# Performance work log

Hardware: AMD Instinct MI355X
Metric: run time of the kernel (lower is better)

Reference implementation:

```python
import jax, jax.numpy as jnp
import numpy as np

N = 50000      # nodes
E = 400000     # edges
HID = 128      # hidden_size
L = 3          # num_att_layer
K = 9          # rbf_size
H = 4          # heads
C = HID // H   # out_channels per head (32)
G = 512        # graphs in batch
CUTOFF = 10.0


def _rbf(D):
    # ExponentialRBF: softplus(softplus_inverse(x)) == x, so centers/widths are the raw values
    centers = jnp.linspace(1.0, float(np.exp(-CUTOFF)), K)          # (K,)
    width = (0.5 / ((1.0 - np.exp(-CUTOFF)) / K)) ** 2              # scalar
    x = D / CUTOFF
    x3 = x ** 3
    x4 = x3 * x
    x5 = x4 * x
    cut = jnp.where(x < 1.0, 1.0 - 6.0 * x5 + 15.0 * x4 - 10.0 * x3, 0.0)
    return cut[:, None] * jnp.exp(-width * (jnp.exp(-D)[:, None] - centers) ** 2)  # (E,K)


def _ln(x, g, b):
    mu = jnp.mean(x, axis=-1, keepdims=True)
    var = jnp.var(x, axis=-1, keepdims=True)
    return (x - mu) / jnp.sqrt(var + 1e-5) * g + b


def _seg_softmax(logits, seg, n):
    # numerically stable softmax over edges grouped by target node
    m = jax.ops.segment_max(logits, seg, num_segments=n)
    e = jnp.exp(logits - m[seg])
    s = jax.ops.segment_sum(e, seg, num_segments=n)
    return e / s[seg]


def setup_inputs() -> dict:
    key = jax.random.key(0)
    ks = jax.random.split(key, 32)
    s = 1.0 / np.sqrt(HID)
    se = 1.0 / np.sqrt(K + 1)
    sb = 1.0 / np.sqrt(3 * HID)
    nrm = jax.random.normal
    inp = {
        "h": nrm(ks[0], (N, HID), jnp.float32),
        "pos": nrm(ks[1], (N, 3), jnp.float32) * 3.0,
        "edge_weight": jax.random.uniform(ks[2], (E,), jnp.float32),
        "Wq": nrm(ks[3], (L, HID, HID)) * s,   "bq": nrm(ks[4], (L, HID)) * 0.01,
        "Wk": nrm(ks[5], (L, HID, HID)) * s,   "bk": nrm(ks[6], (L, HID)) * 0.01,
        "Wv": nrm(ks[7], (L, HID, HID)) * s,   "bv": nrm(ks[8], (L, HID)) * 0.01,
        "We": nrm(ks[9], (L, K + 1, HID)) * se,
        "Wskip": nrm(ks[10], (L, HID, HID)) * s, "bskip": nrm(ks[11], (L, HID)) * 0.01,
        "Wbeta": nrm(ks[12], (L, 3 * HID, 1)) * sb,
        "Wffn1": nrm(ks[13], (L, HID, HID)) * s, "bffn1": nrm(ks[14], (L, HID)) * 0.01,
        "Wffn2": nrm(ks[15], (L, HID, HID)) * s, "bffn2": nrm(ks[16], (L, HID)) * 0.01,
        "Wffn3": nrm(ks[17], (L, HID, HID)) * s, "bffn3": nrm(ks[18], (L, HID)) * 0.01,
        "ln_g": jnp.ones((HID,), jnp.float32),
        "ln_b": jnp.zeros((HID,), jnp.float32),
        "Wo1": nrm(ks[19], (HID, HID)) * s, "bo1": nrm(ks[20], (HID,)) * 0.01,
        "Wo2": nrm(ks[21], (HID, 1)) * s,   "bo2": nrm(ks[22], (1,)) * 0.01,
        "edge_index": jax.random.randint(ks[23], (2, E), 0, N),
        "batch": jnp.sort(jax.random.randint(ks[24], (N,), 0, G)),
    }
    return inp


def reference(h, pos, edge_weight, Wq, bq, Wk, bk, Wv, bv, We, Wskip, bskip, Wbeta,
              Wffn1, bffn1, Wffn2, bffn2, Wffn3, bffn3, ln_g, ln_b, Wo1, bo1, Wo2, bo2,
              edge_index, batch):
    sp = jax.nn.softplus
    n = h.shape[0]
    src, dst = edge_index[0], edge_index[1]  # source j -> target i
    D = jnp.linalg.norm(pos[dst] - pos[src], axis=-1)              # (E,)
    efeat = jnp.concatenate([_rbf(D), edge_weight[:, None]], -1)   # (E, K+1)
    inv_sqrt_c = 1.0 / np.sqrt(C)

    for i in range(L):
        hn = _ln(h, ln_g, ln_b)
        q = (hn @ Wq[i] + bq[i]).reshape(n, H, C)
        k = (hn @ Wk[i] + bk[i]).reshape(n, H, C)
        v = (hn @ Wv[i] + bv[i]).reshape(n, H, C)
        ea = (efeat @ We[i]).reshape(-1, H, C)                     # (E,H,C)
        kj = k[src] + ea
        alpha = jnp.einsum('ehc,ehc->eh', q[dst], kj) * inv_sqrt_c  # (E,H)
        alpha = _seg_softmax(alpha, dst, n)
        # dropout p=0.5 is a no-op in eval mode
        msg = (v[src] + ea) * alpha[:, :, None]
        out = jax.ops.segment_sum(msg, dst, num_segments=n).reshape(n, H * C)
        x_r = hn @ Wskip[i] + bskip[i]
        beta = jax.nn.sigmoid(jnp.concatenate([out, x_r, out - x_r], -1) @ Wbeta[i])
        out = beta * x_r + (1.0 - beta) * out
        h = hn + sp(out)
        hn2 = _ln(h, ln_g, ln_b)
        f = sp(hn2 @ Wffn1[i] + bffn1[i])
        f = sp(f @ Wffn2[i] + bffn2[i])
        f = sp(f @ Wffn3[i] + bffn3[i])
        h = hn2 + f

    pooled = jax.ops.segment_sum(h, batch, num_segments=G)          # (G, HID)
    return sp(pooled @ Wo1 + bo1) @ Wo2 + bo2                       # (G, 1)
```

## Files before the change

### kernel.cpp

```cpp
#include <hip/hip_runtime.h>
#include <hip/hip_bf16.h>
#include <math.h>

#define HID 128
#define KRBF 9
#define NLAYER 3
#define QSSTR 320
#define KVSTR 256
#define QWCOLS 576

typedef __attribute__((ext_vector_type(8))) short bf16x8;
typedef __attribute__((ext_vector_type(4))) float f32x4;

__device__ __forceinline__ float sp_(float x){ return fmaxf(x,0.f) + log1pf(expf(-fabsf(x))); }
__device__ __forceinline__ float sigm_(float x){ return 1.f/(1.f+expf(-x)); }
__device__ __forceinline__ float b2f(short s){
  union{unsigned u; float f;} x; x.u = ((unsigned)(unsigned short)s)<<16; return x.f;
}
__device__ __forceinline__ float wsum64(float v){
  #pragma unroll
  for(int m=1;m<64;m<<=1) v += __shfl_xor(v,m,64);
  return v;
}
__device__ __forceinline__ float wsum16(float v){
  #pragma unroll
  for(int m=1;m<16;m<<=1) v += __shfl_xor(v,m,64);
  return v;
}
__device__ __forceinline__ float2 ldbf2(const __hip_bfloat16* p){
  __hip_bfloat162 b = *(const __hip_bfloat162*)p;
  return make_float2(__bfloat162float(b.x), __bfloat162float(b.y));
}
__device__ __forceinline__ int lb_(const int* __restrict__ a, int n, int key){
  int lo=0, hi=n;
  while(lo<hi){ int mid=(lo+hi)>>1; if(a[mid]<key) lo=mid+1; else hi=mid; }
  return lo;
}

__global__ void count_dst(const int* __restrict__ ei, int* __restrict__ counts, int E){
  int e = blockIdx.x*256+threadIdx.x;
  if(e<E) atomicAdd(&counts[ei[E+e]],1);
}
__global__ void scan1(const int* __restrict__ counts, int* __restrict__ tmp,
                      int* __restrict__ bsums, int N){
  __shared__ int lds[256];
  int t = threadIdx.x; int idx = blockIdx.x*256+t;
  int v = (idx<N)? counts[idx]:0;
  lds[t]=v; __syncthreads();
  for(int off=1;off<256;off<<=1){
    int x = (t>=off)? lds[t-off]:0;
    __syncthreads();
    lds[t]+=x; __syncthreads();
  }
  if(idx<N) tmp[idx]=lds[t];
  if(t==255) bsums[blockIdx.x]=lds[255];
}
__global__ void scan2(const int* __restrict__ bsums, int* __restrict__ boffs, int nb){
  __shared__ int lds[256];
  int t=threadIdx.x;
  int v = (t<nb)? bsums[t]:0;
  lds[t]=v; __syncthreads();
  for(int off=1;off<256;off<<=1){
    int x=(t>=off)?lds[t-off]:0;
    __syncthreads();
    lds[t]+=x; __syncthreads();
  }
  if(t<nb) boffs[t] = lds[t]-v;
}
__global__ void finalize_rs(const int* __restrict__ tmp, const int* __restrict__ boffs,
                            int* __restrict__ row_start, int N){
  int idx = blockIdx.x*256+threadIdx.x;
  if(idx<N) row_start[idx+1] = tmp[idx] + boffs[idx>>8];
  if(idx==0) row_start[0]=0;
}

__global__ void edge_prep(const float* __restrict__ pos, const float* __restrict__ ew,
                          const int* __restrict__ ei, const int* __restrict__ rowst,
                          int* __restrict__ counts2, float* __restrict__ efs,
                          int* __restrict__ esrc, int E){
  int e = blockIdx.x*256 + threadIdx.x;
  if(e>=E) return;
  int s = ei[e], d = ei[E+e];
  float dx = pos[d*3+0]-pos[s*3+0];
  float dy = pos[d*3+1]-pos[s*3+1];
  float dz = pos[d*3+2]-pos[s*3+2];
  float D = sqrtf(dx*dx+dy*dy+dz*dz);
  float x = D*0.1f;
  float cut = 0.f;
  if(x < 1.f){ float x3=x*x*x, x4=x3*x, x5=x4*x; cut = 1.f - 6.f*x5 + 15.f*x4 - 10.f*x3; }
  float ed = expf(-D);
  const double e10 = 4.5399929762484854e-05;
  const float step  = (float)((e10 - 1.0)/8.0);
  const float width = (float)((4.5/(1.0-e10))*(4.5/(1.0-e10)));
  float r12[12];
  #pragma unroll
  for(int k=0;k<KRBF;k++){
    float c = 1.0f + k*step;
    float dd = ed - c;
    r12[k] = cut*expf(-width*dd*dd);
  }
  r12[9] = ew[e]; r12[10]=0.f; r12[11]=0.f;
  int p = rowst[d] + atomicAdd(&counts2[d],1);
  float* o = efs + (size_t)p*12;
  *(float4*)&o[0] = *(float4*)&r12[0];
  *(float4*)&o[4] = *(float4*)&r12[4];
  *(float4*)&o[8] = *(float4*)&r12[8];
  esrc[p] = s;
}

__global__ void pack_w(const float* __restrict__ Wq, const float* __restrict__ Wk,
                       const float* __restrict__ Wv, const float* __restrict__ Wsk,
                       const float* __restrict__ bq, const float* __restrict__ bk,
                       const float* __restrict__ bv, const float* __restrict__ bsk,
                       const float* __restrict__ We,
                       const float* __restrict__ W1, const float* __restrict__ W2,
                       const float* __restrict__ W3,
                       __hip_bfloat16* __restrict__ Wqkvs, float* __restrict__ bqkvs,
                       __hip_bfloat16* __restrict__ Wffn){
  int idx = blockIdx.x*256 + threadIdx.x;
  const int QT = NLAYER*QWCOLS*128;
  const int FT = NLAYER*3*128*128;
  const int BT = NLAYER*QWCOLS;
  if(idx < QT){
    int l = idx / (QWCOLS*128);
    int rem = idx - l*(QWCOLS*128);
    int col = rem >> 7, k = rem & 127;
    float v;
    if(col < 512){
      const float* src = (col<128)?Wq:((col<256)?Wk:((col<384)?Wv:Wsk));
      v = src[(size_t)l*16384 + k*128 + (col&127)];
    } else if(col < 552){
      int j = col-512; int h=j/10; int r=j-10*h;
      const float* wq = Wq + (size_t)l*16384 + k*128;
      const float* we = We + (size_t)l*1280 + r*128;
      float acc=0.f;
      #pragma unroll 8
      for(int c=32*h;c<32*h+32;c++) acc = fmaf(wq[c], we[c], acc);
      v = acc;
    } else v = 0.f;
    Wqkvs[idx] = __float2bfloat16(v);
  } else if(idx < QT+FT){
    int j = idx - QT;
    int k = j & 127; int n = (j>>7)&127; int f = (j>>14)%3; int l = j/(3*16384);
    const float* src = (f==0)?W1:((f==1)?W2:W3);
    Wffn[j] = __float2bfloat16(src[(size_t)l*16384 + k*128 + n]);
  } else if(idx < QT+FT+BT){
    int j = idx - QT - FT;
    int l = j/QWCOLS; int col = j - l*QWCOLS;
    float v;
    if(col<512){
      const float* src = (col<128)?bq:((col<256)?bk:((col<384)?bv:bsk));
      v = src[l*128 + (col&127)];
    } else if(col<552){
      int jj=col-512; int h=jj/10; int r=jj-10*h;
      const float* bqp = bq + l*128;
      const float* we = We + (size_t)l*1280 + r*128;
      float acc=0.f;
      for(int c=32*h;c<32*h+32;c++) acc = fmaf(bqp[c], we[c], acc);
      v = acc;
    } else v = 0.f;
    bqkvs[j] = v;
  }
}

__global__ void ln_node(const float* __restrict__ h, const float* __restrict__ g,
                        const float* __restrict__ b, __hip_bfloat16* __restrict__ hn, int N){
  int n = blockIdx.x*4 + (threadIdx.x>>6);
  if(n>=N) return;
  int lane = threadIdx.x & 63;
  int c = 2*lane;
  float2 v = *(const float2*)&h[(size_t)n*HID + c];
  float s1 = wsum64(v.x+v.y);
  float s2 = wsum64(v.x*v.x+v.y*v.y);
  float mu = s1*(1.f/HID);
  float var = s2*(1.f/HID) - mu*mu;
  float rs = rsqrtf(var + 1e-5f);
  __hip_bfloat162 o;
  o.x = __float2bfloat16((v.x-mu)*rs*g[c]   + b[c]);
  o.y = __float2bfloat16((v.y-mu)*rs*g[c+1] + b[c+1]);
  *(__hip_bfloat162*)&hn[(size_t)n*HID + c] = o;
}

__global__ __launch_bounds__(256) void gemm_mfma(
    const __hip_bfloat16* __restrict__ A, const __hip_bfloat16* __restrict__ Wt,
    const float* __restrict__ bias, const __hip_bfloat16* __restrict__ res,
    void* __restrict__ out0, void* __restrict__ out1,
    const float* __restrict__ lng, const float* __restrict__ lnb,
    int N, int ncols, int mode){
  __shared__ __hip_bfloat16 As[128][136];
  __shared__ __hip_bfloat16 Ws[128][136];
  int row0 = blockIdx.y*128;
  int col0 = blockIdx.x*128;
  int tid = threadIdx.x;
  {
    int chunk = tid&15; int rbase = tid>>4;
    #pragma unroll
    for(int i=0;i<8;i++){
      int r = rbase + 16*i;
      int row = row0 + r;
      float4 v = make_float4(0.f,0.f,0.f,0.f);
      if(row < N) v = *(const float4*)&A[(size_t)row*128 + chunk*8];
      *(float4*)&As[r][chunk*8] = v;
    }
    #pragma unroll
    for(int i=0;i<8;i++){
      int c = rbase + 16*i;
      float4 v = make_float4(0.f,0.f,0.f,0.f);
      if(col0 + c < ncols) v = *(const float4*)&Wt[(size_t)(col0+c)*128 + chunk*8];
      *(float4*)&Ws[c][chunk*8] = v;
    }
  }
  __syncthreads();
  int lane = tid&63;
  int m0 = (tid>>6)*32;
  int ql = lane>>4;
  int il = lane&15;
  f32x4 acc[2][8];
  #pragma unroll
  for(int mi=0;mi<2;mi++)
    #pragma unroll
    for(int nj=0;nj<8;nj++)
      acc[mi][nj] = (f32x4){0.f,0.f,0.f,0.f};
  #pragma unroll
  for(int kk=0;kk<128;kk+=32){
    bf16x8 a0 = *(bf16x8*)&As[m0+il][kk+ql*8];
    bf16x8 a1 = *(bf16x8*)&As[m0+16+il][kk+ql*8];
    bf16x8 bb[8];
    #pragma unroll
    for(int nj=0;nj<8;nj++) bb[nj] = *(bf16x8*)&Ws[nj*16+il][kk+ql*8];
    #pragma unroll
    for(int nj=0;nj<8;nj++){
      acc[0][nj] = __builtin_amdgcn_mfma_f32_16x16x32_bf16(a0, bb[nj], acc[0][nj], 0,0,0);
      acc[1][nj] = __builtin_amdgcn_mfma_f32_16x16x32_bf16(a1, bb[nj], acc[1][nj], 0,0,0);
    }
  }
  if(mode==0){
    __hip_bfloat16* qs  = (__hip_bfloat16*)out0;
    __hip_bfloat16* kvb = (__hip_bfloat16*)out1;
    #pragma unroll
    for(int mi=0;mi<2;mi++){
      int rowb = row0 + m0 + mi*16 + ql*4;
      #pragma unroll
      for(int r=0;r<4;r++){
        int rr = rowb + r;
        if(rr >= N) continue;
        #pragma unroll
        for(int nj=0;nj<8;nj++){
          int cg = col0 + nj*16 + il;
          if(cg >= QWCOLS) continue;
          float t = acc[mi][nj][r] + bias[cg];
          __hip_bfloat16 bv = __float2bfloat16(t);
          if(cg < 128)      qs[(size_t)rr*QSSTR + cg] = bv;
          else if(cg < 384) kvb[(size_t)rr*KVSTR + (cg-128)] = bv;
          else if(cg < 512) qs[(size_t)rr*QSSTR + 128 + (cg-384)] = bv;
          else if(cg < 552) qs[(size_t)rr*QSSTR + 256 + (cg-512)] = bv;
        }
      }
    }
  } else if(mode==1){
    __hip_bfloat16* o = (__hip_bfloat16*)out0;
    #pragma unroll
    for(int mi=0;mi<2;mi++){
      int rowb = row0 + m0 + mi*16 + ql*4;
      #pragma unroll
      for(int r=0;r<4;r++){
        int rr = rowb + r;
        if(rr >= N) continue;
        #pragma unroll
        for(int nj=0;nj<8;nj++){
          int cg = nj*16 + il;
          o[(size_t)rr*128 + cg] = __float2bfloat16(sp_(acc[mi][nj][r] + bias[cg]));
        }
      }
    }
  } else {
    float* hout = (float*)out0;
    __hip_bfloat16* hnout = (__hip_bfloat16*)out1;
    #pragma unroll
    for(int mi=0;mi<2;mi++){
      int rowb = row0 + m0 + mi*16 + ql*4;
      float t[8][4];
      #pragma unroll
      for(int r=0;r<4;r++){
        int rr = rowb + r;
        bool ok = rr < N;
        #pragma unroll
        for(int nj=0;nj<8;nj++){
          int cg = nj*16 + il;
          float x = sp_(acc[mi][nj][r] + bias[cg]);
          float rv = ok ? __bfloat162float(res[(size_t)rr*128 + cg]) : 0.f;
          t[nj][r] = x + rv;
        }
      }
      #pragma unroll
      for(int r=0;r<4;r++){
        int rr = rowb + r;
        if(rr >= N) continue;
        float s1=0.f, s2=0.f;
        #pragma unroll
        for(int nj=0;nj<8;nj++){ float v=t[nj][r]; s1+=v; s2+=v*v; }
        s1 = wsum16(s1); s2 = wsum16(s2);
        float mu = s1*(1.f/128.f);
        float var = s2*(1.f/128.f) - mu*mu;
        float rs = rsqrtf(var + 1e-5f);
        #pragma unroll
        for(int nj=0;nj<8;nj++){
          int cg = nj*16 + il;
          float tv = t[nj][r];
          hout[(size_t)rr*128 + cg] = tv;
          hnout[(size_t)rr*128 + cg] = __float2bfloat16((tv-mu)*rs*lng[cg] + lnb[cg]);
        }
      }
    }
  }
}

__global__ __launch_bounds__(256) void attn_fused2(
    const __hip_bfloat16* __restrict__ qs, const __hip_bfloat16* __restrict__ kvb,
    const float* __restrict__ efs, const int* __restrict__ esrc,
    const float* __restrict__ WeL, const int* __restrict__ rowst,
    float* __restrict__ att, int N){
  int n = blockIdx.x*4 + (threadIdx.x>>6);
  if(n>=N) return;
  int lane = threadIdx.x & 63;
  int eg = lane>>4, sl = lane&15;
  int c8 = sl*8, hd = sl>>2;
  const __hip_bfloat16* rowq = qs + (size_t)n*QSSTR;
  float q8[8];
  {
    bf16x8 qv = *(const bf16x8*)&rowq[c8];
    #pragma unroll
    for(int j=0;j<8;j++) q8[j] = b2f(qv[j]);
  }
  float QW[10];
  #pragma unroll
  for(int r=0;r<10;r++) QW[r] = __bfloat162float(rowq[256 + hd*10 + r]);
  int lo = rowst[n], hi = rowst[n+1];
  float ssum = 0.f;
  float a8[8]; float S[10];
  #pragma unroll
  for(int j=0;j<8;j++) a8[j]=0.f;
  #pragma unroll
  for(int r=0;r<10;r++) S[r]=0.f;
  int i = lo + eg;
  if(i < hi){
    int s = esrc[i];
    const __hip_bfloat16* kr = kvb + (size_t)s*KVSTR;
    bf16x8 kc = *(const bf16x8*)&kr[c8];
    bf16x8 vc = *(const bf16x8*)&kr[128 + c8];
    const float* ef = efs + (size_t)i*12;
    float4 e0 = *(const float4*)&ef[0];
    float4 e1 = *(const float4*)&ef[4];
    float2 e2 = *(const float2*)&ef[8];
    while(true){
      int inext = i + 4;
      bool more = inext < hi;
      bf16x8 kn = kc, vn = vc;
      float4 f0 = e0, f1 = e1; float2 f2 = e2;
      if(more){
        int s2 = esrc[inext];
        const __hip_bfloat16* kr2 = kvb + (size_t)s2*KVSTR;
        kn = *(const bf16x8*)&kr2[c8];
        vn = *(const bf16x8*)&kr2[128 + c8];
        const float* ef2 = efs + (size_t)inext*12;
        f0 = *(const float4*)&ef2[0];
        f1 = *(const float4*)&ef2[4];
        f2 = *(const float2*)&ef2[8];
      }
      float d = 0.f;
      #pragma unroll
      for(int j=0;j<8;j++) d = fmaf(q8[j], b2f(kc[j]), d);
      d += __shfl_xor(d,1,64); d += __shfl_xor(d,2,64);
      float lg = d;
      lg = fmaf(e0.x,QW[0],lg); lg = fmaf(e0.y,QW[1],lg);
      lg = fmaf(e0.z,QW[2],lg); lg = fmaf(e0.w,QW[3],lg);
      lg = fmaf(e1.x,QW[4],lg); lg = fmaf(e1.y,QW[5],lg);
      lg = fmaf(e1.z,QW[6],lg); lg = fmaf(e1.w,QW[7],lg);
      lg = fmaf(e2.x,QW[8],lg); lg = fmaf(e2.y,QW[9],lg);
      lg *= 0.17677669529663687f;
      lg = fminf(lg, 80.f);
      float w = __expf(lg);
      ssum += w;
      #pragma unroll
      for(int j=0;j<8;j++) a8[j] = fmaf(w, b2f(vc[j]), a8[j]);
      S[0]=fmaf(w,e0.x,S[0]); S[1]=fmaf(w,e0.y,S[1]); S[2]=fmaf(w,e0.z,S[2]);
      S[3]=fmaf(w,e0.w,S[3]); S[4]=fmaf(w,e1.x,S[4]); S[5]=fmaf(w,e1.y,S[5]);
      S[6]=fmaf(w,e1.z,S[6]); S[7]=fmaf(w,e1.w,S[7]); S[8]=fmaf(w,e2.x,S[8]);
      S[9]=fmaf(w,e2.y,S[9]);
      if(!more) break;
      kc = kn; vc = vn; e0 = f0; e1 = f1; e2 = f2;
      i = inext;
    }
  }
  #pragma unroll
  for(int m=16;m<64;m<<=1){
    ssum += __shfl_xor(ssum,m,64);
    #pragma unroll
    for(int j=0;j<8;j++) a8[j] += __shfl_xor(a8[j],m,64);
    #pragma unroll
    for(int r=0;r<10;r++) S[r] += __shfl_xor(S[r],m,64);
  }
  float inv = (hi>lo)? 1.f/ssum : 0.f;
  float o8[8];
  #pragma unroll
  for(int j=0;j<8;j++) o8[j]=a8[j];
  #pragma unroll
  for(int r=0;r<10;r++){
    float s=S[r];
    float4 wa = *(const float4*)&WeL[r*128+c8];
    float4 wb = *(const float4*)&WeL[r*128+c8+4];
    o8[0]=fmaf(s,wa.x,o8[0]); o8[1]=fmaf(s,wa.y,o8[1]);
    o8[2]=fmaf(s,wa.z,o8[2]); o8[3]=fmaf(s,wa.w,o8[3]);
    o8[4]=fmaf(s,wb.x,o8[4]); o8[5]=fmaf(s,wb.y,o8[5]);
    o8[6]=fmaf(s,wb.z,o8[6]); o8[7]=fmaf(s,wb.w,o8[7]);
  }
  if(eg==0){
    float4 v0 = make_float4(o8[0]*inv, o8[1]*inv, o8[2]*inv, o8[3]*inv);
    float4 v1 = make_float4(o8[4]*inv, o8[5]*inv, o8[6]*inv, o8[7]*inv);
    *(float4*)&att[(size_t)n*128 + c8]     = v0;
    *(float4*)&att[(size_t)n*128 + c8 + 4] = v1;
  }
}

__global__ void combine_ln(const float* __restrict__ att, const __hip_bfloat16* __restrict__ qs,
                           const __hip_bfloat16* __restrict__ hn, const float* __restrict__ Wb,
                           const float* __restrict__ g, const float* __restrict__ b,
                           __hip_bfloat16* __restrict__ hn2, int N){
  int n = blockIdx.x*4 + (threadIdx.x>>6);
  if(n>=N) return;
  int lane = threadIdx.x&63;
  int c = 2*lane;
  float2 o  = *(const float2*)&att[(size_t)n*HID+c];
  float2 xr = ldbf2(&qs[(size_t)n*QSSTR + 128 + c]);
  float bl = o.x*Wb[c] + o.y*Wb[c+1]
           + xr.x*Wb[HID+c] + xr.y*Wb[HID+c+1]
           + (o.x-xr.x)*Wb[2*HID+c] + (o.y-xr.y)*Wb[2*HID+c+1];
  bl = wsum64(bl);
  float beta = sigm_(bl);
  float u0 = beta*xr.x + (1.f-beta)*o.x;
  float u1 = beta*xr.y + (1.f-beta)*o.y;
  float2 hnv = ldbf2(&hn[(size_t)n*HID+c]);
  float h0 = hnv.x + sp_(u0);
  float h1 = hnv.y + sp_(u1);
  float s1 = wsum64(h0+h1);
  float s2 = wsum64(h0*h0+h1*h1);
  float mu = s1*(1.f/HID);
  float var = s2*(1.f/HID)-mu*mu;
  float rs = rsqrtf(var+1e-5f);
  __hip_bfloat162 outv;
  outv.x = __float2bfloat16((h0-mu)*rs*g[c]+b[c]);
  outv.y = __float2bfloat16((h1-mu)*rs*g[c+1]+b[c+1]);
  *(__hip_bfloat162*)&hn2[(size_t)n*HID+c] = outv;
}

__global__ void pool_head(const float* __restrict__ h, const int* __restrict__ batch,
                          const float* __restrict__ Wo1, const float* __restrict__ bo1,
                          const float* __restrict__ Wo2, const float* __restrict__ bo2,
                          float* __restrict__ out, int N){
  int gid = blockIdx.x;
  int t = threadIdx.x;
  int lo = lb_(batch, N, gid), hi = lb_(batch, N, gid+1);
  __shared__ float pl[128];
  __shared__ float red[128];
  float s = 0.f;
  for(int i=lo;i<hi;i++) s += h[(size_t)i*HID + t];
  pl[t] = s;
  __syncthreads();
  float acc = bo1[t];
  for(int c=0;c<128;c++) acc = fmaf(pl[c], Wo1[c*HID+t], acc);
  red[t] = sp_(acc)*Wo2[t];
  __syncthreads();
  for(int off=64;off>0;off>>=1){
    if(t<off) red[t]+=red[t+off];
    __syncthreads();
  }
  if(t==0) out[gid] = red[0] + bo2[0];
}

extern "C" void kernel_launch(void* const* d_in, const int* in_sizes, int n_in,
                              void* d_out, int out_size, void* d_ws, size_t ws_size,
                              hipStream_t stream){
  const float* h_in = (const float*)d_in[0];
  const float* pos  = (const float*)d_in[1];
  const float* ew   = (const float*)d_in[2];
  const float* Wq = (const float*)d_in[3];  const float* bq = (const float*)d_in[4];
  const float* Wk = (const float*)d_in[5];  const float* bk = (const float*)d_in[6];
  const float* Wv = (const float*)d_in[7];  const float* bv = (const float*)d_in[8];
  const float* We = (const float*)d_in[9];
  const float* Wsk= (const float*)d_in[10]; const float* bsk=(const float*)d_in[11];
  const float* Wbeta=(const float*)d_in[12];
  const float* W1=(const float*)d_in[13]; const float* b1=(const float*)d_in[14];
  const float* W2=(const float*)d_in[15]; const float* b2=(const float*)d_in[16];
  const float* W3=(const float*)d_in[17]; const float* b3=(const float*)d_in[18];
  const float* lng=(const float*)d_in[19]; const float* lnb=(const float*)d_in[20];
  const float* Wo1=(const float*)d_in[21]; const float* bo1=(const float*)d_in[22];
  const float* Wo2=(const float*)d_in[23]; const float* bo2=(const float*)d_in[24];
  const int* ei    = (const int*)d_in[25];
  const int* batch = (const int*)d_in[26];
  int N = in_sizes[0]/HID;
  int E = in_sizes[2];
  int G = out_size;
  float* out = (float*)d_out;

  char* ws = (char*)d_ws;
  size_t off=0;
  auto alloc=[&](size_t bytes)->char*{
    char* p = ws + off;
    off = (off + bytes + 255) & ~(size_t)255;
    return p;
  };
  float* efs   =(float*)alloc((size_t)E*12*4);
  int* esrc    =(int*)  alloc((size_t)E*4);
  int* counts  =(int*)  alloc((size_t)N*4);
  int* counts2 =(int*)  alloc((size_t)N*4);
  int* rowst   =(int*)  alloc((size_t)(N+1)*4);
  int* tmp     =(int*)  alloc((size_t)N*4);
  int* bsums   =(int*)  alloc(256*4);
  int* boffs   =(int*)  alloc(256*4);
  __hip_bfloat16* hn   =(__hip_bfloat16*)alloc((size_t)N*HID*2);
  __hip_bfloat16* hn2  =(__hip_bfloat16*)alloc((size_t)N*HID*2);
  __hip_bfloat16* qsb  =(__hip_bfloat16*)alloc((size_t)N*QSSTR*2);
  __hip_bfloat16* kvb  =(__hip_bfloat16*)alloc((size_t)N*KVSTR*2);
  __hip_bfloat16* f1   =(__hip_bfloat16*)alloc((size_t)N*HID*2);
  __hip_bfloat16* f2   =(__hip_bfloat16*)alloc((size_t)N*HID*2);
  float* att   =(float*)alloc((size_t)N*HID*4);
  float* hcur  =(float*)alloc((size_t)N*HID*4);
  __hip_bfloat16* Wqkvs_t =(__hip_bfloat16*)alloc((size_t)NLAYER*QWCOLS*128*2);
  __hip_bfloat16* Wffn_t  =(__hip_bfloat16*)alloc((size_t)NLAYER*3*128*128*2);
  float* bqkvs =(float*)alloc((size_t)NLAYER*QWCOLS*4);

  int ebl = (E+255)/256;
  int nb  = (N+255)/256;
  int nwb = (N+3)/4;
  int nrb = (N+127)/128;
  dim3 gqkvs((QWCOLS+127)/128, nrb);
  dim3 gffn(1, nrb);

  hipMemsetAsync(counts, 0, (size_t)N*4, stream);
  hipMemsetAsync(counts2,0, (size_t)N*4, stream);
  count_dst<<<ebl,256,0,stream>>>(ei,counts,E);
  scan1<<<nb,256,0,stream>>>(counts,tmp,bsums,N);
  scan2<<<1,256,0,stream>>>(bsums,boffs,nb);
  finalize_rs<<<nb,256,0,stream>>>(tmp,boffs,rowst,N);
  edge_prep<<<ebl,256,0,stream>>>(pos,ew,ei,rowst,counts2,efs,esrc,E);
  {
    int tot = NLAYER*QWCOLS*128 + NLAYER*3*128*128 + NLAYER*QWCOLS;
    pack_w<<<(tot+255)/256,256,0,stream>>>(Wq,Wk,Wv,Wsk,bq,bk,bv,bsk,We,W1,W2,W3,
                                           Wqkvs_t,bqkvs,Wffn_t);
  }

  ln_node<<<nwb,256,0,stream>>>(h_in,lng,lnb,hn,N);
  for(int l=0;l<NLAYER;l++){
    const float* We_l = We + (size_t)l*(KRBF+1)*HID;
    const float* Wb_l = Wbeta + (size_t)l*3*HID;
    const float* b1_l = b1 + (size_t)l*HID;
    const float* b2_l = b2 + (size_t)l*HID;
    const float* b3_l = b3 + (size_t)l*HID;

    gemm_mfma<<<gqkvs,256,0,stream>>>(hn, Wqkvs_t + (size_t)l*QWCOLS*128, bqkvs + l*QWCOLS,
                                      nullptr, qsb, kvb, lng, lnb, N, QWCOLS, 0);
    attn_fused2<<<nwb,256,0,stream>>>(qsb,kvb,efs,esrc,We_l,rowst,att,N);
    combine_ln<<<nwb,256,0,stream>>>(att,qsb,hn,Wb_l,lng,lnb,hn2,N);
    gemm_mfma<<<gffn,256,0,stream>>>(hn2, Wffn_t + (size_t)(l*3+0)*16384, b1_l,
                                     nullptr, f1, nullptr, lng, lnb, N, 128, 1);
    gemm_mfma<<<gffn,256,0,stream>>>(f1,  Wffn_t + (size_t)(l*3+1)*16384, b2_l,
                                     nullptr, f2, nullptr, lng, lnb, N, 128, 1);
    gemm_mfma<<<gffn,256,0,stream>>>(f2,  Wffn_t + (size_t)(l*3+2)*16384, b3_l,
                                     hn2, hcur, hn, lng, lnb, N, 128, 2);
  }
  pool_head<<<G,128,0,stream>>>(hcur,batch,Wo1,bo1,Wo2,bo2,out,N);
}
```

Before: 1.055 ms.

## Permute GEMM weight columns for vector stores and widen attention edge parallelism

Weight columns are packed in a permuted order so each lane's eight MFMA outputs land in contiguous columns. That turns the scattered scalar bf16 epilogue stores into 16-byte vector stores, with the bias and LayerNorm parameters loaded as vectors too. The GEMM is templated on mode and rows per wave, and it loads the A fragments straight from global memory into registers, dropping the shared A tile. The FFN GEMMs use 64-row tiles to launch more blocks. The attention kernel now processes 8 edges per wave at once, with 16 channels per lane instead of a 4-edge software-prefetch loop; this adds register pressure and wastes lanes on low-degree nodes.

```diff
diff --git a/kernel.cpp b/kernel.cpp
--- a/kernel.cpp
+++ b/kernel.cpp
@@ -7,7 +7,7 @@
 #define NLAYER 3
 #define QSSTR 320
 #define KVSTR 256
-#define QWCOLS 576
+#define QWCOLS 640
 
 typedef __attribute__((ext_vector_type(8))) short bf16x8;
 typedef __attribute__((ext_vector_type(4))) float f32x4;
@@ -16,6 +16,10 @@
 __device__ __forceinline__ float sigm_(float x){ return 1.f/(1.f+expf(-x)); }
 __device__ __forceinline__ float b2f(short s){
   union{unsigned u; float f;} x; x.u = ((unsigned)(unsigned short)s)<<16; return x.f;
+}
+__device__ __forceinline__ short f2bs(float x){
+  __hip_bfloat16 b = __float2bfloat16(x);
+  return *reinterpret_cast<short*>(&b);
 }
 __device__ __forceinline__ float wsum64(float v){
   #pragma unroll
@@ -124,30 +128,34 @@
   if(idx < QT){
     int l = idx / (QWCOLS*128);
     int rem = idx - l*(QWCOLS*128);
-    int col = rem >> 7, k = rem & 127;
-    float v;
-    if(col < 512){
-      const float* src = (col<128)?Wq:((col<256)?Wk:((col<384)?Wv:Wsk));
-      v = src[(size_t)l*16384 + k*128 + (col&127)];
-    } else if(col < 552){
-      int j = col-512; int h=j/10; int r=j-10*h;
+    int colp = rem >> 7, k = rem & 127;
+    int b = colp >> 7, p = colp & 127;
+    int g = ((p&15)<<3) + (p>>4);
+    int gcol = b*128 + g;
+    float v = 0.f;
+    if(gcol < 512){
+      const float* src = (gcol<128)?Wq:((gcol<256)?Wk:((gcol<384)?Wv:Wsk));
+      v = src[(size_t)l*16384 + k*128 + (gcol&127)];
+    } else if(gcol < 552){
+      int j = gcol-512; int h=j/10; int r=j-10*h;
       const float* wq = Wq + (size_t)l*16384 + k*128;
       const float* we = We + (size_t)l*1280 + r*128;
       float acc=0.f;
       #pragma unroll 8
       for(int c=32*h;c<32*h+32;c++) acc = fmaf(wq[c], we[c], acc);
       v = acc;
-    } else v = 0.f;
+    }
     Wqkvs[idx] = __float2bfloat16(v);
   } else if(idx < QT+FT){
     int j = idx - QT;
-    int k = j & 127; int n = (j>>7)&127; int f = (j>>14)%3; int l = j/(3*16384);
+    int k = j & 127; int colp = (j>>7)&127; int f = (j>>14)%3; int l = j/(3*16384);
+    int g = ((colp&15)<<3) + (colp>>4);
     const float* src = (f==0)?W1:((f==1)?W2:W3);
-    Wffn[j] = __float2bfloat16(src[(size_t)l*16384 + k*128 + n]);
+    Wffn[j] = __float2bfloat16(src[(size_t)l*16384 + k*128 + g]);
   } else if(idx < QT+FT+BT){
     int j = idx - QT - FT;
     int l = j/QWCOLS; int col = j - l*QWCOLS;
-    float v;
+    float v = 0.f;
     if(col<512){
       const float* src = (col<128)?bq:((col<256)?bk:((col<384)?bv:bsk));
       v = src[l*128 + (col&127)];
@@ -158,7 +166,7 @@
       float acc=0.f;
       for(int c=32*h;c<32*h+32;c++) acc = fmaf(bqp[c], we[c], acc);
       v = acc;
-    } else v = 0.f;
+    }
     bqkvs[j] = v;
   }
 }
@@ -181,141 +189,135 @@
   *(__hip_bfloat162*)&hn[(size_t)n*HID + c] = o;
 }
 
-__global__ __launch_bounds__(256) void gemm_mfma(
+template<int MODE, int MI>
+__global__ __launch_bounds__(256) void gemm_t(
     const __hip_bfloat16* __restrict__ A, const __hip_bfloat16* __restrict__ Wt,
     const float* __restrict__ bias, const __hip_bfloat16* __restrict__ res,
     void* __restrict__ out0, void* __restrict__ out1,
-    const float* __restrict__ lng, const float* __restrict__ lnb,
-    int N, int ncols, int mode){
-  __shared__ __hip_bfloat16 As[128][136];
-  __shared__ __hip_bfloat16 Ws[128][136];
-  int row0 = blockIdx.y*128;
-  int col0 = blockIdx.x*128;
+    const float* __restrict__ lng, const float* __restrict__ lnb, int N){
+  __shared__ __hip_bfloat16 Ws[128][140];
+  int row0 = blockIdx.y*(MI*64);
+  int cb = blockIdx.x;
   int tid = threadIdx.x;
   {
-    int chunk = tid&15; int rbase = tid>>4;
+    int chunk = tid&15, rbase = tid>>4;
     #pragma unroll
     for(int i=0;i<8;i++){
-      int r = rbase + 16*i;
-      int row = row0 + r;
-      float4 v = make_float4(0.f,0.f,0.f,0.f);
-      if(row < N) v = *(const float4*)&A[(size_t)row*128 + chunk*8];
-      *(float4*)&As[r][chunk*8] = v;
-    }
-    #pragma unroll
-    for(int i=0;i<8;i++){
-      int c = rbase + 16*i;
-      float4 v = make_float4(0.f,0.f,0.f,0.f);
-      if(col0 + c < ncols) v = *(const float4*)&Wt[(size_t)(col0+c)*128 + chunk*8];
-      *(float4*)&Ws[c][chunk*8] = v;
-    }
+      int p = rbase + 16*i;
+      *(float4*)&Ws[p][chunk*8] =
+        *(const float4*)&Wt[(size_t)(cb*128+p)*128 + chunk*8];
+    }
+  }
+  int lane = tid&63;
+  int m0 = (tid>>6)*(MI*16);
+  int ql = lane>>4, il = lane&15;
+  bf16x8 af[MI][4];
+  #pragma unroll
+  for(int mi=0;mi<MI;mi++){
+    int r = row0 + m0 + mi*16 + il;
+    r = (r < N) ? r : (N-1);
+    const __hip_bfloat16* ap = A + (size_t)r*128 + ql*8;
+    #pragma unroll
+    for(int kc=0;kc<4;kc++) af[mi][kc] = *(const bf16x8*)(ap + kc*32);
   }
   __syncthreads();
-  int lane = tid&63;
-  int m0 = (tid>>6)*32;
-  int ql = lane>>4;
-  int il = lane&15;
-  f32x4 acc[2][8];
-  #pragma unroll
-  for(int mi=0;mi<2;mi++)
-    #pragma unroll
-    for(int nj=0;nj<8;nj++)
-      acc[mi][nj] = (f32x4){0.f,0.f,0.f,0.f};
-  #pragma unroll
-  for(int kk=0;kk<128;kk+=32){
-    bf16x8 a0 = *(bf16x8*)&As[m0+il][kk+ql*8];
-    bf16x8 a1 = *(bf16x8*)&As[m0+16+il][kk+ql*8];
-    bf16x8 bb[8];
-    #pragma unroll
-    for(int nj=0;nj<8;nj++) bb[nj] = *(bf16x8*)&Ws[nj*16+il][kk+ql*8];
+  f32x4 acc[MI][8];
+  #pragma unroll
+  for(int mi=0;mi<MI;mi++)
+    #pragma unroll
+    for(int nj=0;nj<8;nj++) acc[mi][nj] = (f32x4){0.f,0.f,0.f,0.f};
+  #pragma unroll
+  for(int kc=0;kc<4;kc++){
     #pragma unroll
     for(int nj=0;nj<8;nj++){
-      acc[0][nj] = __builtin_amdgcn_mfma_f32_16x16x32_bf16(a0, bb[nj], acc[0][nj], 0,0,0);
-      acc[1][nj] = __builtin_amdgcn_mfma_f32_16x16x32_bf16(a1, bb[nj], acc[1][nj], 0,0,0);
-    }
-  }
-  if(mode==0){
-    __hip_bfloat16* qs  = (__hip_bfloat16*)out0;
-    __hip_bfloat16* kvb = (__hip_bfloat16*)out1;
-    #pragma unroll
-    for(int mi=0;mi<2;mi++){
-      int rowb = row0 + m0 + mi*16 + ql*4;
+      bf16x8 bb = *(bf16x8*)&Ws[nj*16+il][kc*32+ql*8];
+      #pragma unroll
+      for(int mi=0;mi<MI;mi++)
+        acc[mi][nj] = __builtin_amdgcn_mfma_f32_16x16x32_bf16(af[mi][kc], bb, acc[mi][nj], 0,0,0);
+    }
+  }
+  float bl8[8];
+  {
+    float4 b0 = *(const float4*)&bias[cb*128 + il*8];
+    float4 b1 = *(const float4*)&bias[cb*128 + il*8 + 4];
+    bl8[0]=b0.x; bl8[1]=b0.y; bl8[2]=b0.z; bl8[3]=b0.w;
+    bl8[4]=b1.x; bl8[5]=b1.y; bl8[6]=b1.z; bl8[7]=b1.w;
+  }
+  if(MODE==0){
+    __hip_bfloat16* qsO = (__hip_bfloat16*)out0;
+    __hip_bfloat16* kvO = (__hip_bfloat16*)out1;
+    #pragma unroll
+    for(int mi=0;mi<MI;mi++){
       #pragma unroll
       for(int r=0;r<4;r++){
-        int rr = rowb + r;
+        int rr = row0 + m0 + mi*16 + ql*4 + r;
         if(rr >= N) continue;
+        bf16x8 o;
         #pragma unroll
-        for(int nj=0;nj<8;nj++){
-          int cg = col0 + nj*16 + il;
-          if(cg >= QWCOLS) continue;
-          float t = acc[mi][nj][r] + bias[cg];
-          __hip_bfloat16 bv = __float2bfloat16(t);
-          if(cg < 128)      qs[(size_t)rr*QSSTR + cg] = bv;
-          else if(cg < 384) kvb[(size_t)rr*KVSTR + (cg-128)] = bv;
-          else if(cg < 512) qs[(size_t)rr*QSSTR + 128 + (cg-384)] = bv;
-          else if(cg < 552) qs[(size_t)rr*QSSTR + 256 + (cg-512)] = bv;
-        }
+        for(int nj=0;nj<8;nj++) o[nj] = f2bs(acc[mi][nj][r] + bl8[nj]);
+        __hip_bfloat16* dst; bool ok = true;
+        if(cb==0)      dst = qsO + (size_t)rr*QSSTR + il*8;
+        else if(cb==1) dst = kvO + (size_t)rr*KVSTR + il*8;
+        else if(cb==2) dst = kvO + (size_t)rr*KVSTR + 128 + il*8;
+        else if(cb==3) dst = qsO + (size_t)rr*QSSTR + 128 + il*8;
+        else { dst = qsO + (size_t)rr*QSSTR + 256 + il*8; ok = (il < 5); }
+        if(ok) *(bf16x8*)dst = o;
       }
     }
-  } else if(mode==1){
-    __hip_bfloat16* o = (__hip_bfloat16*)out0;
-    #pragma unroll
-    for(int mi=0;mi<2;mi++){
-      int rowb = row0 + m0 + mi*16 + ql*4;
+  } else if(MODE==1){
+    __hip_bfloat16* o0 = (__hip_bfloat16*)out0;
+    #pragma unroll
+    for(int mi=0;mi<MI;mi++){
       #pragma unroll
       for(int r=0;r<4;r++){
-        int rr = rowb + r;
+        int rr = row0 + m0 + mi*16 + ql*4 + r;
         if(rr >= N) continue;
+        bf16x8 o;
         #pragma unroll
-        for(int nj=0;nj<8;nj++){
-          int cg = nj*16 + il;
-          o[(size_t)rr*128 + cg] = __float2bfloat16(sp_(acc[mi][nj][r] + bias[cg]));
-        }
+        for(int nj=0;nj<8;nj++) o[nj] = f2bs(sp_(acc[mi][nj][r] + bl8[nj]));
+        *(bf16x8*)&o0[(size_t)rr*128 + il*8] = o;
       }
     }
   } else {
     float* hout = (float*)out0;
     __hip_bfloat16* hnout = (__hip_bfloat16*)out1;
-    #pragma unroll
-    for(int mi=0;mi<2;mi++){
-      int rowb = row0 + m0 + mi*16 + ql*4;
-      float t[8][4];
+    float4 lg0 = *(const float4*)&lng[il*8];
+    float4 lg1 = *(const float4*)&lng[il*8+4];
+    float4 lb0 = *(const float4*)&lnb[il*8];
+    float4 lb1 = *(const float4*)&lnb[il*8+4];
+    float lg8[8] = {lg0.x,lg0.y,lg0.z,lg0.w,lg1.x,lg1.y,lg1.z,lg1.w};
+    float lb8[8] = {lb0.x,lb0.y,lb0.z,lb0.w,lb1.x,lb1.y,lb1.z,lb1.w};
+    #pragma unroll
+    for(int mi=0;mi<MI;mi++){
       #pragma unroll
       for(int r=0;r<4;r++){
-        int rr = rowb + r;
-        bool ok = rr < N;
+        int rr = row0 + m0 + mi*16 + ql*4 + r;
+        if(rr >= N) continue;
+        bf16x8 rv = *(const bf16x8*)&res[(size_t)rr*128 + il*8];
+        float t8[8]; float s1=0.f, s2=0.f;
         #pragma unroll
         for(int nj=0;nj<8;nj++){
-          int cg = nj*16 + il;
-          float x = sp_(acc[mi][nj][r] + bias[cg]);
-          float rv = ok ? __bfloat162float(res[(size_t)rr*128 + cg]) : 0.f;
-          t[nj][r] = x + rv;
+          float x = sp_(acc[mi][nj][r] + bl8[nj]) + b2f(rv[nj]);
+          t8[nj] = x; s1 += x; s2 += x*x;
         }
-      }
-      #pragma unroll
-      for(int r=0;r<4;r++){
-        int rr = rowb + r;
-        if(rr >= N) continue;
-        float s1=0.f, s2=0.f;
-        #pragma unroll
-        for(int nj=0;nj<8;nj++){ float v=t[nj][r]; s1+=v; s2+=v*v; }
         s1 = wsum16(s1); s2 = wsum16(s2);
         float mu = s1*(1.f/128.f);
         float var = s2*(1.f/128.f) - mu*mu;
         float rs = rsqrtf(var + 1e-5f);
+        float4 h0 = make_float4(t8[0],t8[1],t8[2],t8[3]);
+        float4 h1 = make_float4(t8[4],t8[5],t8[6],t8[7]);
+        *(float4*)&hout[(size_t)rr*128 + il*8]     = h0;
+        *(float4*)&hout[(size_t)rr*128 + il*8 + 4] = h1;
+        bf16x8 o;
         #pragma unroll
-        for(int nj=0;nj<8;nj++){
-          int cg = nj*16 + il;
-          float tv = t[nj][r];
-          hout[(size_t)rr*128 + cg] = tv;
-          hnout[(size_t)rr*128 + cg] = __float2bfloat16((tv-mu)*rs*lng[cg] + lnb[cg]);
-        }
+        for(int nj=0;nj<8;nj++) o[nj] = f2bs((t8[nj]-mu)*rs*lg8[nj] + lb8[nj]);
+        *(bf16x8*)&hnout[(size_t)rr*128 + il*8] = o;
       }
     }
   }
 }
 
-__global__ __launch_bounds__(256) void attn_fused2(
+__global__ __launch_bounds__(256) void attn_fused3(
     const __hip_bfloat16* __restrict__ qs, const __hip_bfloat16* __restrict__ kvb,
     const float* __restrict__ efs, const int* __restrict__ esrc,
     const float* __restrict__ WeL, const int* __restrict__ rowst,
@@ -323,102 +325,100 @@
   int n = blockIdx.x*4 + (threadIdx.x>>6);
   if(n>=N) return;
   int lane = threadIdx.x & 63;
-  int eg = lane>>4, sl = lane&15;
-  int c8 = sl*8, hd = sl>>2;
+  int eg = lane>>3, sl = lane&7;
+  int c16 = sl*16, hd = sl>>1;
   const __hip_bfloat16* rowq = qs + (size_t)n*QSSTR;
-  float q8[8];
+  float q16[16];
   {
-    bf16x8 qv = *(const bf16x8*)&rowq[c8];
-    #pragma unroll
-    for(int j=0;j<8;j++) q8[j] = b2f(qv[j]);
+    bf16x8 qa = *(const bf16x8*)&rowq[c16];
+    bf16x8 qb = *(const bf16x8*)&rowq[c16+8];
+    #pragma unroll
+    for(int j=0;j<8;j++){ q16[j] = b2f(qa[j]); q16[8+j] = b2f(qb[j]); }
   }
   float QW[10];
   #pragma unroll
   for(int r=0;r<10;r++) QW[r] = __bfloat162float(rowq[256 + hd*10 + r]);
   int lo = rowst[n], hi = rowst[n+1];
-  float ssum = 0.f;
-  float a8[8]; float S[10];
-  #pragma unroll
-  for(int j=0;j<8;j++) a8[j]=0.f;
+  float ssum = 0.f, a16[16], S[10];
+  #pragma unroll
+  for(int j=0;j<16;j++) a16[j]=0.f;
   #pragma unroll
   for(int r=0;r<10;r++) S[r]=0.f;
-  int i = lo + eg;
-  if(i < hi){
+  for(int i=lo+eg; i<hi; i+=8){
     int s = esrc[i];
     const __hip_bfloat16* kr = kvb + (size_t)s*KVSTR;
-    bf16x8 kc = *(const bf16x8*)&kr[c8];
-    bf16x8 vc = *(const bf16x8*)&kr[128 + c8];
+    bf16x8 ka = *(const bf16x8*)&kr[c16];
+    bf16x8 kb = *(const bf16x8*)&kr[c16+8];
+    bf16x8 va = *(const bf16x8*)&kr[128+c16];
+    bf16x8 vb = *(const bf16x8*)&kr[128+c16+8];
     const float* ef = efs + (size_t)i*12;
     float4 e0 = *(const float4*)&ef[0];
     float4 e1 = *(const float4*)&ef[4];
     float2 e2 = *(const float2*)&ef[8];
-    while(true){
-      int inext = i + 4;
-      bool more = inext < hi;
-      bf16x8 kn = kc, vn = vc;
-      float4 f0 = e0, f1 = e1; float2 f2 = e2;
-      if(more){
-        int s2 = esrc[inext];
-        const __hip_bfloat16* kr2 = kvb + (size_t)s2*KVSTR;
-        kn = *(const bf16x8*)&kr2[c8];
-        vn = *(const bf16x8*)&kr2[128 + c8];
-        const float* ef2 = efs + (size_t)inext*12;
-        f0 = *(const float4*)&ef2[0];
-        f1 = *(const float4*)&ef2[4];
-        f2 = *(const float2*)&ef2[8];
-      }
-      float d = 0.f;
-      #pragma unroll
-      for(int j=0;j<8;j++) d = fmaf(q8[j], b2f(kc[j]), d);
-      d += __shfl_xor(d,1,64); d += __shfl_xor(d,2,64);
-      float lg = d;
-      lg = fmaf(e0.x,QW[0],lg); lg = fmaf(e0.y,QW[1],lg);
-      lg = fmaf(e0.z,QW[2],lg); lg = fmaf(e0.w,QW[3],lg);
-      lg = fmaf(e1.x,QW[4],lg); lg = fmaf(e1.y,QW[5],lg);
-      lg = fmaf(e1.z,QW[6],lg); lg = fmaf(e1.w,QW[7],lg);
-      lg = fmaf(e2.x,QW[8],lg); lg = fmaf(e2.y,QW[9],lg);
-      lg *= 0.17677669529663687f;
-      lg = fminf(lg, 80.f);
-      float w = __expf(lg);
-      ssum += w;
-      #pragma unroll
-      for(int j=0;j<8;j++) a8[j] = fmaf(w, b2f(vc[j]), a8[j]);
-      S[0]=fmaf(w,e0.x,S[0]); S[1]=fmaf(w,e0.y,S[1]); S[2]=fmaf(w,e0.z,S[2]);
-      S[3]=fmaf(w,e0.w,S[3]); S[4]=fmaf(w,e1.x,S[4]); S[5]=fmaf(w,e1.y,S[5]);
-      S[6]=fmaf(w,e1.z,S[6]); S[7]=fmaf(w,e1.w,S[7]); S[8]=fmaf(w,e2.x,S[8]);
-      S[9]=fmaf(w,e2.y,S[9]);
-      if(!more) break;
-      kc = kn; vc = vn; e0 = f0; e1 = f1; e2 = f2;
-      i = inext;
-    }
-  }
-  #pragma unroll
-  for(int m=16;m<64;m<<=1){
+    float d = 0.f;
+    #pragma unroll
+    for(int j=0;j<8;j++){
+      d = fmaf(q16[j],   b2f(ka[j]), d);
+      d = fmaf(q16[8+j], b2f(kb[j]), d);
+    }
+    d += __shfl_xor(d,1,64);
+    float lg = d;
+    lg = fmaf(e0.x,QW[0],lg); lg = fmaf(e0.y,QW[1],lg);
+    lg = fmaf(e0.z,QW[2],lg); lg = fmaf(e0.w,QW[3],lg);
+    lg = fmaf(e1.x,QW[4],lg); lg = fmaf(e1.y,QW[5],lg);
+    lg = fmaf(e1.z,QW[6],lg); lg = fmaf(e1.w,QW[7],lg);
+    lg = fmaf(e2.x,QW[8],lg); lg = fmaf(e2.y,QW[9],lg);
+    lg *= 0.17677669529663687f;
+    lg = fminf(lg, 80.f);
+    float w = __expf(lg);
+    ssum += w;
+    #pragma unroll
+    for(int j=0;j<8;j++){
+      a16[j]   = fmaf(w, b2f(va[j]), a16[j]);
+      a16[8+j] = fmaf(w, b2f(vb[j]), a16[8+j]);
+    }
+    S[0]=fmaf(w,e0.x,S[0]); S[1]=fmaf(w,e0.y,S[1]); S[2]=fmaf(w,e0.z,S[2]);
+    S[3]=fmaf(w,e0.w,S[3]); S[4]=fmaf(w,e1.x,S[4]); S[5]=fmaf(w,e1.y,S[5]);
+    S[6]=fmaf(w,e1.z,S[6]); S[7]=fmaf(w,e1.w,S[7]); S[8]=fmaf(w,e2.x,S[8]);
+    S[9]=fmaf(w,e2.y,S[9]);
+  }
+  #pragma unroll
+  for(int m=8;m<64;m<<=1){
     ssum += __shfl_xor(ssum,m,64);
     #pragma unroll
-    for(int j=0;j<8;j++) a8[j] += __shfl_xor(a8[j],m,64);
+    for(int j=0;j<16;j++) a16[j] += __shfl_xor(a16[j],m,64);
     #pragma unroll
     for(int r=0;r<10;r++) S[r] += __shfl_xor(S[r],m,64);
   }
-  float inv = (hi>lo)? 1.f/ssum : 0.f;
-  float o8[8];
-  #pragma unroll
-  for(int j=0;j<8;j++) o8[j]=a8[j];
-  #pragma unroll
-  for(int r=0;r<10;r++){
-    float s=S[r];
-    float4 wa = *(const float4*)&WeL[r*128+c8];
-    float4 wb = *(const float4*)&WeL[r*128+c8+4];
-    o8[0]=fmaf(s,wa.x,o8[0]); o8[1]=fmaf(s,wa.y,o8[1]);
-    o8[2]=fmaf(s,wa.z,o8[2]); o8[3]=fmaf(s,wa.w,o8[3]);
-    o8[4]=fmaf(s,wb.x,o8[4]); o8[5]=fmaf(s,wb.y,o8[5]);
-    o8[6]=fmaf(s,wb.z,o8[6]); o8[7]=fmaf(s,wb.w,o8[7]);
-  }
   if(eg==0){
-    float4 v0 = make_float4(o8[0]*inv, o8[1]*inv, o8[2]*inv, o8[3]*inv);
-    float4 v1 = make_float4(o8[4]*inv, o8[5]*inv, o8[6]*inv, o8[7]*inv);
-    *(float4*)&att[(size_t)n*128 + c8]     = v0;
-    *(float4*)&att[(size_t)n*128 + c8 + 4] = v1;
+    float inv = (hi>lo)? 1.f/ssum : 0.f;
+    float o16[16];
+    #pragma unroll
+    for(int j=0;j<16;j++) o16[j]=a16[j];
+    #pragma unroll
+    for(int r=0;r<10;r++){
+      float s=S[r];
+      const float* wp = &WeL[r*128 + c16];
+      float4 w0 = *(const float4*)&wp[0];
+      float4 w1 = *(const float4*)&wp[4];
+      float4 w2 = *(const float4*)&wp[8];
+      float4 w3 = *(const float4*)&wp[12];
+      o16[0]=fmaf(s,w0.x,o16[0]);  o16[1]=fmaf(s,w0.y,o16[1]);
+      o16[2]=fmaf(s,w0.z,o16[2]);  o16[3]=fmaf(s,w0.w,o16[3]);
+      o16[4]=fmaf(s,w1.x,o16[4]);  o16[5]=fmaf(s,w1.y,o16[5]);
+      o16[6]=fmaf(s,w1.z,o16[6]);  o16[7]=fmaf(s,w1.w,o16[7]);
+      o16[8]=fmaf(s,w2.x,o16[8]);  o16[9]=fmaf(s,w2.y,o16[9]);
+      o16[10]=fmaf(s,w2.z,o16[10]); o16[11]=fmaf(s,w2.w,o16[11]);
+      o16[12]=fmaf(s,w3.x,o16[12]); o16[13]=fmaf(s,w3.y,o16[13]);
+      o16[14]=fmaf(s,w3.z,o16[14]); o16[15]=fmaf(s,w3.w,o16[15]);
+    }
+    float* ap = att + (size_t)n*128 + c16;
+    #pragma unroll
+    for(int q4=0;q4<4;q4++){
+      float4 v = make_float4(o16[q4*4]*inv, o16[q4*4+1]*inv,
+                             o16[q4*4+2]*inv, o16[q4*4+3]*inv);
+      *(float4*)&ap[q4*4] = v;
+    }
   }
 }
 
@@ -532,9 +532,10 @@
   int ebl = (E+255)/256;
   int nb  = (N+255)/256;
   int nwb = (N+3)/4;
-  int nrb = (N+127)/128;
-  dim3 gqkvs((QWCOLS+127)/128, nrb);
-  dim3 gffn(1, nrb);
+  int nrb128 = (N+127)/128;
+  int nrb64  = (N+63)/64;
+  dim3 gqkvs(QWCOLS/128, nrb128);
+  dim3 gffn(1, nrb64);
 
   hipMemsetAsync(counts, 0, (size_t)N*4, stream);
   hipMemsetAsync(counts2,0, (size_t)N*4, stream);
@@ -557,16 +558,17 @@
     const float* b2_l = b2 + (size_t)l*HID;
     const float* b3_l = b3 + (size_t)l*HID;
 
-    gemm_mfma<<<gqkvs,256,0,stream>>>(hn, Wqkvs_t + (size_t)l*QWCOLS*128, bqkvs + l*QWCOLS,
-                                      nullptr, qsb, kvb, lng, lnb, N, QWCOLS, 0);
-    attn_fused2<<<nwb,256,0,stream>>>(qsb,kvb,efs,esrc,We_l,rowst,att,N);
+    gemm_t<0,2><<<gqkvs,256,0,stream>>>(hn, Wqkvs_t + (size_t)l*QWCOLS*128,
+                                        bqkvs + l*QWCOLS, nullptr, qsb, kvb,
+                                        lng, lnb, N);
+    attn_fused3<<<nwb,256,0,stream>>>(qsb,kvb,efs,esrc,We_l,rowst,att,N);
     combine_ln<<<nwb,256,0,stream>>>(att,qsb,hn,Wb_l,lng,lnb,hn2,N);
-    gemm_mfma<<<gffn,256,0,stream>>>(hn2, Wffn_t + (size_t)(l*3+0)*16384, b1_l,
-                                     nullptr, f1, nullptr, lng, lnb, N, 128, 1);
-    gemm_mfma<<<gffn,256,0,stream>>>(f1,  Wffn_t + (size_t)(l*3+1)*16384, b2_l,
-                                     nullptr, f2, nullptr, lng, lnb, N, 128, 1);
-    gemm_mfma<<<gffn,256,0,stream>>>(f2,  Wffn_t + (size_t)(l*3+2)*16384, b3_l,
-                                     hn2, hcur, hn, lng, lnb, N, 128, 2);
+    gemm_t<1,1><<<gffn,256,0,stream>>>(hn2, Wffn_t + (size_t)(l*3+0)*16384, b1_l,
+                                       nullptr, f1, nullptr, lng, lnb, N);
+    gemm_t<1,1><<<gffn,256,0,stream>>>(f1,  Wffn_t + (size_t)(l*3+1)*16384, b2_l,
+                                       nullptr, f2, nullptr, lng, lnb, N);
+    gemm_t<2,1><<<gffn,256,0,stream>>>(f2,  Wffn_t + (size_t)(l*3+2)*16384, b3_l,
+                                       hn2, hcur, hn, lng, lnb, N);
   }
   pool_head<<<G,128,0,stream>>>(hcur,batch,Wo1,bo1,Wo2,bo2,out,N);
 }
```

New measurement: 961.8 us. 8.9% less time.
